# Optimization experiments

Measured on AMD Instinct MI355X. Metric: run time of the kernel, lower is better.

## Reference

```python
import jax, jax.numpy as jnp
import numpy as np

B, N, D = 4, 1024, 256  # D <= N required by the original indexing trick


def setup_inputs() -> dict:
    key = jax.random.key(0)
    x = jax.random.uniform(key, (B, N, D), dtype=jnp.float32)
    # torch.nonzero(x > 0.5, as_tuple=True): row-major edge order, same as jnp.nonzero
    eb, ei, ej = jnp.nonzero(x > 0.5)  # eager: data-dependent edge count E
    return {"x": x, "eb": eb, "ei": ei, "ej": ej}


def reference(x, eb, ei, ej):
    # Original math: gather ||x[b, e2] - x[b, e1]|| for every (b,e1,e2) with
    # We compute distances only for qualifying edges instead of the dense
    # [B,N,8,N,D] intermediate the torch code materializes.
    diff = x[eb, ei] - x[eb, ej]                      # [E, D] (norm is symmetric in e1,e2)
    s = jnp.sum(diff * diff, axis=-1)                 # [E]
    d = jnp.abs(jnp.sqrt(s))                          # vector_norm then abs (no-op on >=0)
    E = d.shape[0]
    return jnp.broadcast_to(d[:, None, None, None], (E, 8, 1, 1))
```

## Files before the change

### kernel.cpp

```cpp
#include <hip/hip_runtime.h>

#define B_DIM 4
#define N_DIM 1024
#define D_DIM 256

typedef __bf16 bf16x8 __attribute__((ext_vector_type(8)));
typedef float  f32x4  __attribute__((ext_vector_type(4)));

__global__ __launch_bounds__(256) void gram_dist_kernel(
    const float* __restrict__ x, float* __restrict__ Dtab)
{
    const int b  = blockIdx.z;
    const int i0 = blockIdx.y * 64;
    const int j0 = blockIdx.x * 64;
    const float* __restrict__ Xb = x + (size_t)b * N_DIM * D_DIM;

    const int lane = (int)(threadIdx.x & 63u);
    const int wid  = (int)(threadIdx.x >> 6);
    const int im0  = i0 + (wid >> 1) * 32;
    const int jm0  = j0 + (wid & 1) * 32;

    const int rsel = lane & 15;
    const int kg   = lane >> 4;

    f32x4 acc[2][2] = {};
    float na[2] = {0.f, 0.f};
    float nb[2] = {0.f, 0.f};

    for (int k0 = 0; k0 < D_DIM; k0 += 32) {
        bf16x8 af[2], bf[2];
        #pragma unroll
        for (int f = 0; f < 2; ++f) {
            const float* rp = Xb + (size_t)(im0 + f * 16 + rsel) * D_DIM + k0 + kg * 8;
            float4 v0 = *(const float4*)rp;
            float4 v1 = *(const float4*)(rp + 4);
            af[f][0]=(__bf16)v0.x; af[f][1]=(__bf16)v0.y; af[f][2]=(__bf16)v0.z; af[f][3]=(__bf16)v0.w;
            af[f][4]=(__bf16)v1.x; af[f][5]=(__bf16)v1.y; af[f][6]=(__bf16)v1.z; af[f][7]=(__bf16)v1.w;
            na[f] += v0.x*v0.x + v0.y*v0.y + v0.z*v0.z + v0.w*v0.w
                   + v1.x*v1.x + v1.y*v1.y + v1.z*v1.z + v1.w*v1.w;
        }
        #pragma unroll
        for (int f = 0; f < 2; ++f) {
            const float* rp = Xb + (size_t)(jm0 + f * 16 + rsel) * D_DIM + k0 + kg * 8;
            float4 v0 = *(const float4*)rp;
            float4 v1 = *(const float4*)(rp + 4);
            bf[f][0]=(__bf16)v0.x; bf[f][1]=(__bf16)v0.y; bf[f][2]=(__bf16)v0.z; bf[f][3]=(__bf16)v0.w;
            bf[f][4]=(__bf16)v1.x; bf[f][5]=(__bf16)v1.y; bf[f][6]=(__bf16)v1.z; bf[f][7]=(__bf16)v1.w;
            nb[f] += v0.x*v0.x + v0.y*v0.y + v0.z*v0.z + v0.w*v0.w
                   + v1.x*v1.x + v1.y*v1.y + v1.z*v1.z + v1.w*v1.w;
        }
        #pragma unroll
        for (int fm = 0; fm < 2; ++fm)
            #pragma unroll
            for (int fn = 0; fn < 2; ++fn)
                acc[fm][fn] = __builtin_amdgcn_mfma_f32_16x16x32_bf16(
                    af[fm], bf[fn], acc[fm][fn], 0, 0, 0);
    }

    #pragma unroll
    for (int f = 0; f < 2; ++f) {
        na[f] += __shfl_xor(na[f], 16, 64);
        na[f] += __shfl_xor(na[f], 32, 64);
        nb[f] += __shfl_xor(nb[f], 16, 64);
        nb[f] += __shfl_xor(nb[f], 32, 64);
    }

    #pragma unroll
    for (int fm = 0; fm < 2; ++fm) {
        #pragma unroll
        for (int fn = 0; fn < 2; ++fn) {
            const int col = jm0 + fn * 16 + rsel;
            const float nj = nb[fn];
            #pragma unroll
            for (int r = 0; r < 4; ++r) {
                const int r16 = kg * 4 + r;
                const int row = im0 + fm * 16 + r16;
                const float ni = __shfl(na[fm], r16, 64);
                float d2 = ni + nj - 2.0f * acc[fm][fn][r];
                float d  = sqrtf(fmaxf(d2, 0.0f));
                if (row == col) d = 0.0f;
                Dtab[((size_t)b * N_DIM + row) * D_DIM + col] = d;
            }
        }
    }
}

__global__ __launch_bounds__(256) void edge_out_kernel(
    const int* __restrict__ eb, const int* __restrict__ ei,
    const int* __restrict__ ej, const float* __restrict__ Dtab,
    float* __restrict__ out, int E)
{
    const int t = blockIdx.x * 256 + (int)threadIdx.x;
    const int e = t >> 1;
    if (e >= E) return;
    const float d = Dtab[((size_t)eb[e] * N_DIM + ei[e]) * D_DIM + ej[e]];
    *(float4*)(out + (size_t)e * 8 + (t & 1) * 4) = make_float4(d, d, d, d);
}

__global__ __launch_bounds__(256) void edge_dist_direct_kernel(
    const float* __restrict__ x,
    const int* __restrict__ eb, const int* __restrict__ ei,
    const int* __restrict__ ej, float* __restrict__ out, int E)
{
    const int wave = (int)((blockIdx.x * (unsigned)blockDim.x + threadIdx.x) >> 6);
    if (wave >= E) return;
    const int lane = (int)(threadIdx.x & 63u);
    const int b = eb[wave], i = ei[wave], j = ej[wave];
    const float4 a = reinterpret_cast<const float4*>(x + ((size_t)b * N_DIM + i) * D_DIM)[lane];
    const float4 c = reinterpret_cast<const float4*>(x + ((size_t)b * N_DIM + j) * D_DIM)[lane];
    const float dx = a.x - c.x, dy = a.y - c.y, dz = a.z - c.z, dw = a.w - c.w;
    float s = dx * dx + dy * dy + dz * dz + dw * dw;
    #pragma unroll
    for (int off = 32; off >= 1; off >>= 1) s += __shfl_xor(s, off, 64);
    const float d = sqrtf(s);
    if (lane < 2)
        reinterpret_cast<float4*>(out + (size_t)wave * 8)[lane] =
            make_float4(d, d, d, d);
}

extern "C" void kernel_launch(void* const* d_in, const int* in_sizes, int n_in,
                              void* d_out, int out_size, void* d_ws, size_t ws_size,
                              hipStream_t stream) {
    const float* x  = (const float*)d_in[0];
    const int*   eb = (const int*)d_in[1];
    const int*   ei = (const int*)d_in[2];
    const int*   ej = (const int*)d_in[3];
    float* out = (float*)d_out;
    const int E = in_sizes[1];
    if (E <= 0) return;

    const size_t dtab_bytes = (size_t)B_DIM * N_DIM * D_DIM * sizeof(float);

    if (ws_size >= dtab_bytes) {
        float* Dtab = (float*)d_ws;
        dim3 ggrid(D_DIM / 64, N_DIM / 64, B_DIM);
        gram_dist_kernel<<<ggrid, 256, 0, stream>>>(x, Dtab);
        const int threads = 2 * E;
        edge_out_kernel<<<(threads + 255) / 256, 256, 0, stream>>>(eb, ei, ej, Dtab, out, E);
    } else {
        const int blocks = (E + 3) / 4;
        edge_dist_direct_kernel<<<blocks, 256, 0, stream>>>(x, eb, ei, ej, out, E);
    }
}
```

Before: 25.53 us.

## Fuse Gram distance tile with edge scatter via LDS and per-row edge offsets

Replaces the global distance table and the separate edge gather kernel. A small kernel binary-searches the sorted edge list to find where each (b,i) row starts. A fused kernel then computes a 16x256 distance tile with MFMA, stores it in LDS, and writes the outputs for that row range straight from shared memory. This removes the 4 MB table write and its random gather reads, at the cost of an extra launch, a binary-search pass, and only 256 blocks each holding a larger tile.

Result: slower. 36.33 us (+42.3%).

```diff
diff --git a/kernel.cpp b/kernel.cpp
--- a/kernel.cpp
+++ b/kernel.cpp
@@ -3,98 +3,115 @@
 #define B_DIM 4
 #define N_DIM 1024
 #define D_DIM 256
+#define NROWS (B_DIM * N_DIM)
+#define ITILE 16
+#define LDPAD 4
 
 typedef __bf16 bf16x8 __attribute__((ext_vector_type(8)));
 typedef float  f32x4  __attribute__((ext_vector_type(4)));
 
-__global__ __launch_bounds__(256) void gram_dist_kernel(
-    const float* __restrict__ x, float* __restrict__ Dtab)
+__global__ __launch_bounds__(256) void row_start_kernel(
+    const int* __restrict__ eb, const int* __restrict__ ei,
+    int* __restrict__ row_start, int E)
 {
-    const int b  = blockIdx.z;
-    const int i0 = blockIdx.y * 64;
-    const int j0 = blockIdx.x * 64;
+    const int r = blockIdx.x * 256 + (int)threadIdx.x;
+    if (r > NROWS) return;
+    int lo = 0, hi = E;
+    while (lo < hi) {
+        const int mid = (lo + hi) >> 1;
+        const int key = eb[mid] * N_DIM + ei[mid];
+        if (key < r) lo = mid + 1; else hi = mid;
+    }
+    row_start[r] = lo;
+}
+
+__global__ __launch_bounds__(256) void fused_dist_scatter_kernel(
+    const float* __restrict__ x,
+    const int* __restrict__ ei, const int* __restrict__ ej,
+    const int* __restrict__ row_start,
+    float* __restrict__ out)
+{
+    const int bid = (int)blockIdx.x;
+    const int b   = bid >> 6;
+    const int i0  = (bid & 63) * ITILE;
     const float* __restrict__ Xb = x + (size_t)b * N_DIM * D_DIM;
+
+    __shared__ float d_lds[ITILE][D_DIM + LDPAD];
 
     const int lane = (int)(threadIdx.x & 63u);
     const int wid  = (int)(threadIdx.x >> 6);
-    const int im0  = i0 + (wid >> 1) * 32;
-    const int jm0  = j0 + (wid & 1) * 32;
+    const int jbase = wid * 64;
 
     const int rsel = lane & 15;
     const int kg   = lane >> 4;
 
-    f32x4 acc[2][2] = {};
-    float na[2] = {0.f, 0.f};
-    float nb[2] = {0.f, 0.f};
+    f32x4 acc[4] = {};
+    float na = 0.f;
+    float nb[4] = {0.f, 0.f, 0.f, 0.f};
 
     for (int k0 = 0; k0 < D_DIM; k0 += 32) {
-        bf16x8 af[2], bf[2];
-        #pragma unroll
-        for (int f = 0; f < 2; ++f) {
-            const float* rp = Xb + (size_t)(im0 + f * 16 + rsel) * D_DIM + k0 + kg * 8;
+        bf16x8 af;
+        {
+            const float* rp = Xb + (size_t)(i0 + rsel) * D_DIM + k0 + kg * 8;
             float4 v0 = *(const float4*)rp;
             float4 v1 = *(const float4*)(rp + 4);
-            af[f][0]=(__bf16)v0.x; af[f][1]=(__bf16)v0.y; af[f][2]=(__bf16)v0.z; af[f][3]=(__bf16)v0.w;
-            af[f][4]=(__bf16)v1.x; af[f][5]=(__bf16)v1.y; af[f][6]=(__bf16)v1.z; af[f][7]=(__bf16)v1.w;
-            na[f] += v0.x*v0.x + v0.y*v0.y + v0.z*v0.z + v0.w*v0.w
-                   + v1.x*v1.x + v1.y*v1.y + v1.z*v1.z + v1.w*v1.w;
+            af[0]=(__bf16)v0.x; af[1]=(__bf16)v0.y; af[2]=(__bf16)v0.z; af[3]=(__bf16)v0.w;
+            af[4]=(__bf16)v1.x; af[5]=(__bf16)v1.y; af[6]=(__bf16)v1.z; af[7]=(__bf16)v1.w;
+            na += v0.x*v0.x + v0.y*v0.y + v0.z*v0.z + v0.w*v0.w
+                + v1.x*v1.x + v1.y*v1.y + v1.z*v1.z + v1.w*v1.w;
         }
+        bf16x8 bfrag[4];
         #pragma unroll
-        for (int f = 0; f < 2; ++f) {
-            const float* rp = Xb + (size_t)(jm0 + f * 16 + rsel) * D_DIM + k0 + kg * 8;
+        for (int f = 0; f < 4; ++f) {
+            const float* rp = Xb + (size_t)(jbase + f * 16 + rsel) * D_DIM + k0 + kg * 8;
             float4 v0 = *(const float4*)rp;
             float4 v1 = *(const float4*)(rp + 4);
-            bf[f][0]=(__bf16)v0.x; bf[f][1]=(__bf16)v0.y; bf[f][2]=(__bf16)v0.z; bf[f][3]=(__bf16)v0.w;
-            bf[f][4]=(__bf16)v1.x; bf[f][5]=(__bf16)v1.y; bf[f][6]=(__bf16)v1.z; bf[f][7]=(__bf16)v1.w;
+            bfrag[f][0]=(__bf16)v0.x; bfrag[f][1]=(__bf16)v0.y; bfrag[f][2]=(__bf16)v0.z; bfrag[f][3]=(__bf16)v0.w;
+            bfrag[f][4]=(__bf16)v1.x; bfrag[f][5]=(__bf16)v1.y; bfrag[f][6]=(__bf16)v1.z; bfrag[f][7]=(__bf16)v1.w;
             nb[f] += v0.x*v0.x + v0.y*v0.y + v0.z*v0.z + v0.w*v0.w
                    + v1.x*v1.x + v1.y*v1.y + v1.z*v1.z + v1.w*v1.w;
         }
         #pragma unroll
-        for (int fm = 0; fm < 2; ++fm)
-            #pragma unroll
-            for (int fn = 0; fn < 2; ++fn)
-                acc[fm][fn] = __builtin_amdgcn_mfma_f32_16x16x32_bf16(
-                    af[fm], bf[fn], acc[fm][fn], 0, 0, 0);
+        for (int f = 0; f < 4; ++f)
+            acc[f] = __builtin_amdgcn_mfma_f32_16x16x32_bf16(af, bfrag[f], acc[f], 0, 0, 0);
     }
 
+    na += __shfl_xor(na, 16, 64);
+    na += __shfl_xor(na, 32, 64);
     #pragma unroll
-    for (int f = 0; f < 2; ++f) {
-        na[f] += __shfl_xor(na[f], 16, 64);
-        na[f] += __shfl_xor(na[f], 32, 64);
+    for (int f = 0; f < 4; ++f) {
         nb[f] += __shfl_xor(nb[f], 16, 64);
         nb[f] += __shfl_xor(nb[f], 32, 64);
     }
 
     #pragma unroll
-    for (int fm = 0; fm < 2; ++fm) {
+    for (int f = 0; f < 4; ++f) {
+        const int col = jbase + f * 16 + rsel;
+        const float nj = nb[f];
         #pragma unroll
-        for (int fn = 0; fn < 2; ++fn) {
-            const int col = jm0 + fn * 16 + rsel;
-            const float nj = nb[fn];
-            #pragma unroll
-            for (int r = 0; r < 4; ++r) {
-                const int r16 = kg * 4 + r;
-                const int row = im0 + fm * 16 + r16;
-                const float ni = __shfl(na[fm], r16, 64);
-                float d2 = ni + nj - 2.0f * acc[fm][fn][r];
-                float d  = sqrtf(fmaxf(d2, 0.0f));
-                if (row == col) d = 0.0f;
-                Dtab[((size_t)b * N_DIM + row) * D_DIM + col] = d;
-            }
+        for (int r = 0; r < 4; ++r) {
+            const int rloc = kg * 4 + r;
+            const float ni = __shfl(na, rloc, 64);
+            float d2 = ni + nj - 2.0f * acc[f][r];
+            float d  = sqrtf(fmaxf(d2, 0.0f));
+            if (i0 + rloc == col) d = 0.0f;
+            d_lds[rloc][col] = d;
         }
     }
-}
+    __syncthreads();
 
-__global__ __launch_bounds__(256) void edge_out_kernel(
-    const int* __restrict__ eb, const int* __restrict__ ei,
-    const int* __restrict__ ej, const float* __restrict__ Dtab,
-    float* __restrict__ out, int E)
-{
-    const int t = blockIdx.x * 256 + (int)threadIdx.x;
-    const int e = t >> 1;
-    if (e >= E) return;
-    const float d = Dtab[((size_t)eb[e] * N_DIM + ei[e]) * D_DIM + ej[e]];
-    *(float4*)(out + (size_t)e * 8 + (t & 1) * 4) = make_float4(d, d, d, d);
+    const int r0     = b * N_DIM + i0;
+    const int estart = row_start[r0];
+    const int eend   = row_start[r0 + ITILE];
+    for (int e = estart + (int)threadIdx.x; e < eend; e += 256) {
+        const int iloc = ei[e] - i0;
+        const int j    = ej[e];
+        const float d  = d_lds[iloc][j];
+        const float4 v = make_float4(d, d, d, d);
+        float* op = out + (size_t)e * 8;
+        *(float4*)op       = v;
+        *(float4*)(op + 4) = v;
+    }
 }
 
 __global__ __launch_bounds__(256) void edge_dist_direct_kernel(
@@ -129,14 +146,12 @@
     const int E = in_sizes[1];
     if (E <= 0) return;
 
-    const size_t dtab_bytes = (size_t)B_DIM * N_DIM * D_DIM * sizeof(float);
+    const size_t rs_bytes = (size_t)(NROWS + 1) * sizeof(int);
 
-    if (ws_size >= dtab_bytes) {
-        float* Dtab = (float*)d_ws;
-        dim3 ggrid(D_DIM / 64, N_DIM / 64, B_DIM);
-        gram_dist_kernel<<<ggrid, 256, 0, stream>>>(x, Dtab);
-        const int threads = 2 * E;
-        edge_out_kernel<<<(threads + 255) / 256, 256, 0, stream>>>(eb, ei, ej, Dtab, out, E);
+    if (ws_size >= rs_bytes) {
+        int* row_start = (int*)d_ws;
+        row_start_kernel<<<(NROWS + 1 + 255) / 256, 256, 0, stream>>>(eb, ei, row_start, E);
+        fused_dist_scatter_kernel<<<256, 256, 0, stream>>>(x, ei, ej, row_start, out);
     } else {
         const int blocks = (E + 3) / 4;
         edge_dist_direct_kernel<<<blocks, 256, 0, stream>>>(x, eb, ei, ej, out, E);
```

## Stage bf16 row tiles in LDS once and compute norms by coalesced reductions

Applied to the files above, without the earlier changes.

The Gram-distance kernel now loads each 64-row A and B tile once with coalesced float4 reads, converts it to bf16 into padded shared memory, and computes row norms with wave reductions. The MFMA loop then reads its fragments from LDS instead of repeating strided global loads per wave. This is meant to cut redundant global traffic and per-wave conversion work, at the cost of about 66KB of LDS per block, which lowers occupancy, plus a barrier that serializes loading and compute.

New measurement: 28.68 us. 1.12x slower.

```diff
diff --git a/kernel.cpp b/kernel.cpp
--- a/kernel.cpp
+++ b/kernel.cpp
@@ -3,83 +3,88 @@
 #define B_DIM 4
 #define N_DIM 1024
 #define D_DIM 256
+#define NROWS (B_DIM * N_DIM)
+#define LDT 264
 
 typedef __bf16 bf16x8 __attribute__((ext_vector_type(8)));
+typedef __bf16 bf16x4 __attribute__((ext_vector_type(4)));
 typedef float  f32x4  __attribute__((ext_vector_type(4)));
 
-__global__ __launch_bounds__(256) void gram_dist_kernel(
+__global__ __launch_bounds__(256) void gram_dtab_kernel(
     const float* __restrict__ x, float* __restrict__ Dtab)
 {
-    const int b  = blockIdx.z;
-    const int i0 = blockIdx.y * 64;
-    const int j0 = blockIdx.x * 64;
+    const int j0 = (int)blockIdx.x * 64;
+    const int i0 = (int)blockIdx.y * 64;
+    const int b  = (int)blockIdx.z;
     const float* __restrict__ Xb = x + (size_t)b * N_DIM * D_DIM;
 
-    const int lane = (int)(threadIdx.x & 63u);
-    const int wid  = (int)(threadIdx.x >> 6);
-    const int im0  = i0 + (wid >> 1) * 32;
-    const int jm0  = j0 + (wid & 1) * 32;
+    __shared__ __bf16 Asl[64 * LDT];
+    __shared__ __bf16 Bsl[64 * LDT];
+    __shared__ float  na_lds[64];
+    __shared__ float  nb_lds[64];
 
+    const int t  = (int)threadIdx.x;
+    const int w  = t >> 6;
+    const int lq = t & 63;
+
+    #pragma unroll
+    for (int rep = 0; rep < 16; ++rep) {
+        const int row = rep * 4 + w;
+        const float4 v = *(const float4*)(Xb + (size_t)(i0 + row) * D_DIM + lq * 4);
+        bf16x4 h;
+        h[0] = (__bf16)v.x; h[1] = (__bf16)v.y; h[2] = (__bf16)v.z; h[3] = (__bf16)v.w;
+        *(bf16x4*)&Asl[row * LDT + lq * 4] = h;
+        float s = v.x*v.x + v.y*v.y + v.z*v.z + v.w*v.w;
+        #pragma unroll
+        for (int off = 32; off >= 1; off >>= 1) s += __shfl_xor(s, off, 64);
+        if (lq == 0) na_lds[row] = s;
+    }
+    #pragma unroll
+    for (int rep = 0; rep < 16; ++rep) {
+        const int row = rep * 4 + w;
+        const float4 v = *(const float4*)(Xb + (size_t)(j0 + row) * D_DIM + lq * 4);
+        bf16x4 h;
+        h[0] = (__bf16)v.x; h[1] = (__bf16)v.y; h[2] = (__bf16)v.z; h[3] = (__bf16)v.w;
+        *(bf16x4*)&Bsl[row * LDT + lq * 4] = h;
+        float s = v.x*v.x + v.y*v.y + v.z*v.z + v.w*v.w;
+        #pragma unroll
+        for (int off = 32; off >= 1; off >>= 1) s += __shfl_xor(s, off, 64);
+        if (lq == 0) nb_lds[row] = s;
+    }
+    __syncthreads();
+
+    const int lane = t & 63;
+    const int wm   = w >> 1, wn = w & 1;
     const int rsel = lane & 15;
     const int kg   = lane >> 4;
 
     f32x4 acc[2][2] = {};
-    float na[2] = {0.f, 0.f};
-    float nb[2] = {0.f, 0.f};
-
+    #pragma unroll
     for (int k0 = 0; k0 < D_DIM; k0 += 32) {
-        bf16x8 af[2], bf[2];
-        #pragma unroll
-        for (int f = 0; f < 2; ++f) {
-            const float* rp = Xb + (size_t)(im0 + f * 16 + rsel) * D_DIM + k0 + kg * 8;
-            float4 v0 = *(const float4*)rp;
-            float4 v1 = *(const float4*)(rp + 4);
-            af[f][0]=(__bf16)v0.x; af[f][1]=(__bf16)v0.y; af[f][2]=(__bf16)v0.z; af[f][3]=(__bf16)v0.w;
-            af[f][4]=(__bf16)v1.x; af[f][5]=(__bf16)v1.y; af[f][6]=(__bf16)v1.z; af[f][7]=(__bf16)v1.w;
-            na[f] += v0.x*v0.x + v0.y*v0.y + v0.z*v0.z + v0.w*v0.w
-                   + v1.x*v1.x + v1.y*v1.y + v1.z*v1.z + v1.w*v1.w;
-        }
-        #pragma unroll
-        for (int f = 0; f < 2; ++f) {
-            const float* rp = Xb + (size_t)(jm0 + f * 16 + rsel) * D_DIM + k0 + kg * 8;
-            float4 v0 = *(const float4*)rp;
-            float4 v1 = *(const float4*)(rp + 4);
-            bf[f][0]=(__bf16)v0.x; bf[f][1]=(__bf16)v0.y; bf[f][2]=(__bf16)v0.z; bf[f][3]=(__bf16)v0.w;
-            bf[f][4]=(__bf16)v1.x; bf[f][5]=(__bf16)v1.y; bf[f][6]=(__bf16)v1.z; bf[f][7]=(__bf16)v1.w;
-            nb[f] += v0.x*v0.x + v0.y*v0.y + v0.z*v0.z + v0.w*v0.w
-                   + v1.x*v1.x + v1.y*v1.y + v1.z*v1.z + v1.w*v1.w;
-        }
-        #pragma unroll
-        for (int fm = 0; fm < 2; ++fm)
-            #pragma unroll
-            for (int fn = 0; fn < 2; ++fn)
-                acc[fm][fn] = __builtin_amdgcn_mfma_f32_16x16x32_bf16(
-                    af[fm], bf[fn], acc[fm][fn], 0, 0, 0);
-    }
-
-    #pragma unroll
-    for (int f = 0; f < 2; ++f) {
-        na[f] += __shfl_xor(na[f], 16, 64);
-        na[f] += __shfl_xor(na[f], 32, 64);
-        nb[f] += __shfl_xor(nb[f], 16, 64);
-        nb[f] += __shfl_xor(nb[f], 32, 64);
+        const bf16x8 a0 = *(const bf16x8*)&Asl[(wm*32 +      rsel) * LDT + k0 + kg*8];
+        const bf16x8 a1 = *(const bf16x8*)&Asl[(wm*32 + 16 + rsel) * LDT + k0 + kg*8];
+        const bf16x8 b0 = *(const bf16x8*)&Bsl[(wn*32 +      rsel) * LDT + k0 + kg*8];
+        const bf16x8 b1 = *(const bf16x8*)&Bsl[(wn*32 + 16 + rsel) * LDT + k0 + kg*8];
+        acc[0][0] = __builtin_amdgcn_mfma_f32_16x16x32_bf16(a0, b0, acc[0][0], 0, 0, 0);
+        acc[0][1] = __builtin_amdgcn_mfma_f32_16x16x32_bf16(a0, b1, acc[0][1], 0, 0, 0);
+        acc[1][0] = __builtin_amdgcn_mfma_f32_16x16x32_bf16(a1, b0, acc[1][0], 0, 0, 0);
+        acc[1][1] = __builtin_amdgcn_mfma_f32_16x16x32_bf16(a1, b1, acc[1][1], 0, 0, 0);
     }
 
     #pragma unroll
     for (int fm = 0; fm < 2; ++fm) {
         #pragma unroll
         for (int fn = 0; fn < 2; ++fn) {
-            const int col = jm0 + fn * 16 + rsel;
-            const float nj = nb[fn];
+            const int ccol = wn*32 + fn*16 + rsel;
+            const float nj = nb_lds[ccol];
             #pragma unroll
             for (int r = 0; r < 4; ++r) {
-                const int r16 = kg * 4 + r;
-                const int row = im0 + fm * 16 + r16;
-                const float ni = __shfl(na[fm], r16, 64);
+                const int crow = wm*32 + fm*16 + kg*4 + r;
+                const float ni = na_lds[crow];
                 float d2 = ni + nj - 2.0f * acc[fm][fn][r];
                 float d  = sqrtf(fmaxf(d2, 0.0f));
-                if (row == col) d = 0.0f;
-                Dtab[((size_t)b * N_DIM + row) * D_DIM + col] = d;
+                if (i0 + crow == j0 + ccol) d = 0.0f;
+                Dtab[((size_t)b * N_DIM + i0 + crow) * D_DIM + (j0 + ccol)] = d;
             }
         }
     }
@@ -90,7 +95,7 @@
     const int* __restrict__ ej, const float* __restrict__ Dtab,
     float* __restrict__ out, int E)
 {
-    const int t = blockIdx.x * 256 + (int)threadIdx.x;
+    const int t = (int)blockIdx.x * 256 + (int)threadIdx.x;
     const int e = t >> 1;
     if (e >= E) return;
     const float d = Dtab[((size_t)eb[e] * N_DIM + ei[e]) * D_DIM + ej[e]];
@@ -129,12 +134,12 @@
     const int E = in_sizes[1];
     if (E <= 0) return;
 
-    const size_t dtab_bytes = (size_t)B_DIM * N_DIM * D_DIM * sizeof(float);
+    const size_t dtab_bytes = (size_t)NROWS * D_DIM * sizeof(float);
 
     if (ws_size >= dtab_bytes) {
         float* Dtab = (float*)d_ws;
         dim3 ggrid(D_DIM / 64, N_DIM / 64, B_DIM);
-        gram_dist_kernel<<<ggrid, 256, 0, stream>>>(x, Dtab);
+        gram_dtab_kernel<<<ggrid, 256, 0, stream>>>(x, Dtab);
         const int threads = 2 * E;
         edge_out_kernel<<<(threads + 255) / 256, 256, 0, stream>>>(eb, ei, ej, Dtab, out, E);
     } else {
```
